# Kernel tuning notes

Measured on AMD Instinct MI355X. Metric: run time of the kernel, lower is better.

The kernel has to match this reference:

```python
import jax, jax.numpy as jnp
import numpy as np

F_IN, F_OUT, N_HEADS = 64, 256, 4
HEAD_DIM = F_OUT // N_HEADS


def setup_inputs() -> dict:
    key = jax.random.key(0)
    ks = jax.random.split(key, 9)
    s_in = 1.0 / np.sqrt(F_IN)
    s_out = 1.0 / np.sqrt(F_OUT)
    return {
        "x": jax.random.normal(ks[0], (4, 32, F_IN, 512), dtype=jnp.float32),
        "Wq": jax.random.normal(ks[1], (F_IN, F_OUT), dtype=jnp.float32) * s_in,
        "bq": jax.random.normal(ks[2], (F_OUT,), dtype=jnp.float32) * 0.01,
        "Wk": jax.random.normal(ks[3], (F_IN, F_OUT), dtype=jnp.float32) * s_in,
        "bk": jax.random.normal(ks[4], (F_OUT,), dtype=jnp.float32) * 0.01,
        "Wv": jax.random.normal(ks[5], (F_IN, F_OUT), dtype=jnp.float32) * s_in,
        "bv": jax.random.normal(ks[6], (F_OUT,), dtype=jnp.float32) * 0.01,
        "Wo": jax.random.normal(ks[7], (F_OUT, F_OUT), dtype=jnp.float32) * s_out,
        "bo": jax.random.normal(ks[8], (F_OUT,), dtype=jnp.float32) * 0.01,
    }


def reference(x, Wq, bq, Wk, bk, Wv, bv, Wo, bo):
    B, N, Fdim, T = x.shape
    xp = jnp.transpose(x, (0, 1, 3, 2))  # [B, N, T, F]
    q = xp @ Wq + bq  # [B, N, T, f_out]
    k = xp @ Wk + bk
    v = xp @ Wv + bv
    # split f_out into heads: [B, N, T, H, hd]
    q = q.reshape(B, N, T, N_HEADS, HEAD_DIM)
    k = k.reshape(B, N, T, N_HEADS, HEAD_DIM)
    v = v.reshape(B, N, T, N_HEADS, HEAD_DIM)
    scale = 1.0 / np.sqrt(HEAD_DIM)
    # full TxT score matrix per (batch, node, head), as in the original
    scores = jnp.einsum("bnqhd,bnkhd->bnhqk", q, k) * scale
    attn = jax.nn.softmax(scores, axis=-1)
    out = jnp.einsum("bnhqk,bnkhd->bnqhd", attn, v)  # [B, N, T, H, hd]
    out = out.reshape(B, N, T, F_OUT)  # head-concat along feature dim
    out = out @ Wo + bo  # fc_out; dropout is identity at inference
    return jnp.transpose(out, (0, 1, 3, 2))  # [B, N, f_out, T]
```

## Files before the change

kernel.cpp:

```cpp
#include <hip/hip_runtime.h>

constexpr int kT = 512;
constexpr int kF = 64;
constexpr int kC = 256;
constexpr int kH = 4;
constexpr int kHD = 64;
constexpr int kBN = 128;

typedef __attribute__((ext_vector_type(4))) float f32x4;
typedef __attribute__((ext_vector_type(8))) short s16x8;
typedef __attribute__((ext_vector_type(4))) unsigned int u32x4;

__device__ inline unsigned short f2bf(float f) {
  unsigned int u = __float_as_uint(f);
  u += 0x7fff + ((u >> 16) & 1);
  return (unsigned short)(u >> 16);
}

__device__ inline float max3f(float a, float b, float c) {
  return fmaxf(fmaxf(a, b), c);
}

__device__ inline float exp2_hw(float x) {
  float r;
  asm("v_exp_f32 %0, %1" : "=v"(r) : "v"(x));
  return r;
}

__global__ __launch_bounds__(256) void k_prep(
    const float* __restrict__ Wq, const float* __restrict__ Wk,
    const float* __restrict__ Wv, const float* __restrict__ Wo,
    unsigned short* __restrict__ WB, unsigned short* __restrict__ WoT) {
  int i = blockIdx.x * 256 + threadIdx.x;
  const int total = 768 * 64 + 256 * 256;
  for (; i < total; i += gridDim.x * 256) {
    if (i < 768 * 64) {
      int c = i >> 6, f = i & 63;
      int arr = c >> 8, cc = c & 255;
      const float* W = (arr == 0) ? Wq : (arr == 1) ? Wk : Wv;
      WB[i] = f2bf(W[f * 256 + cc]);
    } else {
      int j = i - 768 * 64;
      int co = j >> 8, c = j & 255;
      WoT[j] = f2bf(Wo[c * 256 + co]);
    }
  }
}

__global__ __launch_bounds__(256) void k_qkv(
    const float* __restrict__ x, const unsigned short* __restrict__ WB,
    const float* __restrict__ bq, const float* __restrict__ bk,
    const float* __restrict__ bv,
    unsigned short* __restrict__ Qw, unsigned short* __restrict__ Kw,
    unsigned short* __restrict__ Vw, int bn0) {
  __shared__ __align__(16) unsigned short shm[9216];

  const int tid = threadIdx.x;
  const int lbn = blockIdx.x >> 2;
  const int tch = blockIdx.x & 3;
  const float* xb = x + (size_t)(bn0 + lbn) * kF * kT + tch * 128;

  for (int idx = tid; idx < 2048; idx += 256) {
    int f = idx >> 5, t4 = idx & 31;
    float4 v = *(const float4*)(xb + f * kT + t4 * 4);
    shm[(t4 * 4 + 0) * 72 + f] = f2bf(v.x);
    shm[(t4 * 4 + 1) * 72 + f] = f2bf(v.y);
    shm[(t4 * 4 + 2) * 72 + f] = f2bf(v.z);
    shm[(t4 * 4 + 3) * 72 + f] = f2bf(v.w);
  }
  __syncthreads();

  const int lane = tid & 63, wid = tid >> 6;
  const int lr = lane & 15, lg = lane >> 4;

  s16x8 bfr[8][2];
#pragma unroll
  for (int tj = 0; tj < 8; ++tj)
#pragma unroll
    for (int kk = 0; kk < 2; ++kk)
      bfr[tj][kk] = *(const s16x8*)&shm[(tj * 16 + lr) * 72 + kk * 32 + lg * 8];
  __syncthreads();

  const float kQscale = 0.180336880111120426f;

  for (int i = 0; i < 12; ++i) {
    const int ci = wid * 12 + i;
    const int c0 = ci * 16;
    s16x8 af0 = *(const s16x8*)(WB + (size_t)(c0 + lr) * 64 + lg * 8);
    s16x8 af1 = *(const s16x8*)(WB + (size_t)(c0 + lr) * 64 + 32 + lg * 8);

    f32x4 acc[8];
#pragma unroll
    for (int tj = 0; tj < 8; ++tj) {
      f32x4 a = {0.f, 0.f, 0.f, 0.f};
      a = __builtin_amdgcn_mfma_f32_16x16x32_bf16(af0, bfr[tj][0], a, 0, 0, 0);
      a = __builtin_amdgcn_mfma_f32_16x16x32_bf16(af1, bfr[tj][1], a, 0, 0, 0);
      acc[tj] = a;
    }

    const int arr = c0 >> 8;
    const int h = (c0 & 255) >> 6;
    const int dbase0 = (c0 & 63);
    const int dbase = dbase0 + lg * 4;
    const float* bsrc = (arr == 0) ? bq : (arr == 1) ? bk : bv;
    float b0 = bsrc[h * 64 + dbase + 0];
    float b1 = bsrc[h * 64 + dbase + 1];
    float b2 = bsrc[h * 64 + dbase + 2];
    float b3 = bsrc[h * 64 + dbase + 3];

    if (arr < 2) {
      const float scale = (arr == 0) ? kQscale : 1.0f;
      unsigned short* dst = ((arr == 0) ? Qw : Kw) +
                            (size_t)(lbn * kH + h) * kT * kHD;
#pragma unroll
      for (int tj = 0; tj < 8; ++tj) {
        int t = tch * 128 + tj * 16 + lr;
        float v0 = (acc[tj][0] + b0) * scale;
        float v1 = (acc[tj][1] + b1) * scale;
        float v2 = (acc[tj][2] + b2) * scale;
        float v3 = (acc[tj][3] + b3) * scale;
        unsigned long long pk =
            (unsigned long long)f2bf(v0) |
            ((unsigned long long)f2bf(v1) << 16) |
            ((unsigned long long)f2bf(v2) << 32) |
            ((unsigned long long)f2bf(v3) << 48);
        *(unsigned long long*)(dst + (size_t)t * kHD + dbase) = pk;
      }
    } else {
      unsigned short* buf = shm + wid * (16 * 144);
#pragma unroll
      for (int tj = 0; tj < 8; ++tj) {
        buf[(lg * 4 + 0) * 144 + tj * 16 + lr] = f2bf(acc[tj][0] + b0);
        buf[(lg * 4 + 1) * 144 + tj * 16 + lr] = f2bf(acc[tj][1] + b1);
        buf[(lg * 4 + 2) * 144 + tj * 16 + lr] = f2bf(acc[tj][2] + b2);
        buf[(lg * 4 + 3) * 144 + tj * 16 + lr] = f2bf(acc[tj][3] + b3);
      }
      asm volatile("s_waitcnt lgkmcnt(0)" ::: "memory");
      unsigned short* dst = Vw + (size_t)(lbn * kH + h) * kHD * kT;
      const int row = lane >> 2, cc = lane & 3;
#pragma unroll
      for (int q4 = 0; q4 < 4; ++q4) {
        uint4 vv = *(const uint4*)&buf[row * 144 + (q4 * 4 + cc) * 8];
        *(uint4*)(dst + (size_t)(dbase0 + row) * kT + tch * 128 +
                  (q4 * 4 + cc) * 8) = vv;
      }
    }
  }
}

__global__ __launch_bounds__(1024, 4) void k_attn(
    const unsigned short* __restrict__ Qw, const unsigned short* __restrict__ Kw,
    const unsigned short* __restrict__ Vw, unsigned short* __restrict__ Aw) {
  __shared__ __align__(16) unsigned char KlB[512 * 128];
  __shared__ __align__(16) unsigned char VtB[64 * 1024];

  const int tid = threadIdx.x;
  const int lbn = blockIdx.x >> 2;
  const int h = blockIdx.x & 3;
  const size_t hb = (size_t)(lbn * kH + h) * kT * kHD;

  const uint4* Ksrc = (const uint4*)(Kw + hb);
#pragma unroll
  for (int i = 0; i < 4; ++i) {
    int cidx = tid + i * 1024;
    int t = cidx >> 3, c8 = cidx & 7;
    *(uint4*)(KlB + ((t * 128 + c8 * 16) ^ ((t & 7) << 4))) = Ksrc[cidx];
  }
  const unsigned short* Vs = Vw + hb;
#pragma unroll
  for (int i = 0; i < 8; ++i) {
    int gi = tid + i * 1024;
    int d = gi >> 7, gr = gi & 127;
    int b32 = gr >> 3, g2 = gr & 7;
    int hh = g2 >> 1, e = g2 & 1;
    uint2 v = *(const uint2*)(Vs + d * 512 + b32 * 32 + e * 16 + hh * 4);
    *(uint2*)(VtB + ((d * 1024 + gr * 8) ^ ((d & 7) << 4))) = v;
  }
  __syncthreads();

  const int lane = tid & 63, wid = tid >> 6;
  const int lr = lane & 15, lg = lane >> 4;
  const int swz = (lr & 7) << 4;
  const unsigned short* Qb = Qw + hb;
  unsigned short* Ab = Aw + (size_t)lbn * kT * kC + h * kHD;

  const int qbase = wid * 32;
  s16x8 qf[2][2];
#pragma unroll
  for (int qt = 0; qt < 2; ++qt) {
    qf[qt][0] = *(const s16x8*)(Qb + (size_t)(qbase + qt * 16 + lr) * kHD + lg * 8);
    qf[qt][1] = *(const s16x8*)(Qb + (size_t)(qbase + qt * 16 + lr) * kHD + 32 + lg * 8);
  }

  f32x4 o0[4] = {{0,0,0,0},{0,0,0,0},{0,0,0,0},{0,0,0,0}};
  f32x4 o1[4] = {{0,0,0,0},{0,0,0,0},{0,0,0,0},{0,0,0,0}};
  float m0 = -3e38f, m1 = -3e38f, l0 = 0.f, l1 = 0.f;

  const int koff = (lg * 16) ^ swz;
  const unsigned char* kp0 = KlB + lr * 128 + koff;
  const unsigned char* kp1 = KlB + lr * 128 + (koff ^ 64);
  const int voff = (lg * 16) ^ swz;
  const unsigned char* vp0 = VtB + lr * 1024 + voff;
  const unsigned char* vp1 = VtB + lr * 1024 + (voff ^ 64);

  unsigned int w0[8], w1[8];

#define SOFTMAX_QT(sa, m, l, o, w)                                            \
  {                                                                           \
    float g0 = max3f(sa[0][0], sa[0][1], sa[0][2]);                           \
    float g1 = max3f(sa[0][3], sa[1][0], sa[1][1]);                           \
    float g2 = max3f(sa[1][2], sa[1][3], sa[2][0]);                           \
    float g3 = max3f(sa[2][1], sa[2][2], sa[2][3]);                           \
    float g4 = max3f(sa[3][0], sa[3][1], sa[3][2]);                           \
    float tm = fmaxf(max3f(g0, g1, g2), max3f(g3, g4, sa[3][3]));             \
    if (__any(tm > m + 8.0f)) {                                               \
      tm = fmaxf(tm, __shfl_xor(tm, 16));                                     \
      tm = fmaxf(tm, __shfl_xor(tm, 32));                                     \
      float mn = fmaxf(m, tm);                                                \
      float al = exp2_hw(m - mn);                                             \
      m = mn;                                                                 \
      l *= al;                                                                \
      float aq0 = __shfl(al, (lane & 48) | (lg * 4 + 0));                     \
      float aq1 = __shfl(al, (lane & 48) | (lg * 4 + 1));                     \
      float aq2 = __shfl(al, (lane & 48) | (lg * 4 + 2));                     \
      float aq3 = __shfl(al, (lane & 48) | (lg * 4 + 3));                     \
      _Pragma("unroll")                                                       \
      for (int dt = 0; dt < 4; ++dt) {                                        \
        o[dt][0] *= aq0; o[dt][1] *= aq1;                                     \
        o[dt][2] *= aq2; o[dt][3] *= aq3;                                     \
      }                                                                       \
    }                                                                         \
    _Pragma("unroll")                                                         \
    for (int s = 0; s < 4; ++s) {                                             \
      float e0 = exp2_hw(sa[s][0] - m);                                       \
      float e1 = exp2_hw(sa[s][1] - m);                                       \
      float e2 = exp2_hw(sa[s][2] - m);                                       \
      float e3 = exp2_hw(sa[s][3] - m);                                       \
      l += (e0 + e1) + (e2 + e3);                                             \
      asm("v_cvt_pk_bf16_f32 %0, %1, %2" : "=v"(w[2*s]) : "v"(e0), "v"(e1));  \
      asm("v_cvt_pk_bf16_f32 %0, %1, %2" : "=v"(w[2*s+1]) : "v"(e2), "v"(e3));\
    }                                                                         \
  }

  for (int kc = 0; kc < 8; ++kc) {
    f32x4 sa0[4], sa1[4];
#pragma unroll
    for (int s = 0; s < 4; ++s) {
      s16x8 kf0 = *(const s16x8*)(kp0 + s * 2048);
      s16x8 kf1 = *(const s16x8*)(kp1 + s * 2048);
      f32x4 z0 = {0.f, 0.f, 0.f, 0.f};
      z0 = __builtin_amdgcn_mfma_f32_16x16x32_bf16(kf0, qf[0][0], z0, 0, 0, 0);
      z0 = __builtin_amdgcn_mfma_f32_16x16x32_bf16(kf1, qf[0][1], z0, 0, 0, 0);
      sa0[s] = z0;
      f32x4 z1 = {0.f, 0.f, 0.f, 0.f};
      z1 = __builtin_amdgcn_mfma_f32_16x16x32_bf16(kf0, qf[1][0], z1, 0, 0, 0);
      z1 = __builtin_amdgcn_mfma_f32_16x16x32_bf16(kf1, qf[1][1], z1, 0, 0, 0);
      sa1[s] = z1;
    }
    kp0 += 8192;
    kp1 += 8192;

    SOFTMAX_QT(sa0, m0, l0, o0, w0)
    SOFTMAX_QT(sa1, m1, l1, o1, w1)

    s16x8 pa00 = __builtin_bit_cast(s16x8, (u32x4){w0[0], w0[1], w0[2], w0[3]});
    s16x8 pa01 = __builtin_bit_cast(s16x8, (u32x4){w0[4], w0[5], w0[6], w0[7]});
    s16x8 pa10 = __builtin_bit_cast(s16x8, (u32x4){w1[0], w1[1], w1[2], w1[3]});
    s16x8 pa11 = __builtin_bit_cast(s16x8, (u32x4){w1[4], w1[5], w1[6], w1[7]});

#pragma unroll
    for (int dt = 0; dt < 4; ++dt) {
      s16x8 vb = *(const s16x8*)(vp0 + dt * 16384);
      o0[dt] = __builtin_amdgcn_mfma_f32_16x16x32_bf16(pa00, vb, o0[dt], 0, 0, 0);
      o1[dt] = __builtin_amdgcn_mfma_f32_16x16x32_bf16(pa10, vb, o1[dt], 0, 0, 0);
    }
#pragma unroll
    for (int dt = 0; dt < 4; ++dt) {
      s16x8 vb = *(const s16x8*)(vp1 + dt * 16384);
      o0[dt] = __builtin_amdgcn_mfma_f32_16x16x32_bf16(pa01, vb, o0[dt], 0, 0, 0);
      o1[dt] = __builtin_amdgcn_mfma_f32_16x16x32_bf16(pa11, vb, o1[dt], 0, 0, 0);
    }
    vp0 += 128;
    vp1 += 128;
  }
#undef SOFTMAX_QT

#pragma unroll
  for (int qt = 0; qt < 2; ++qt) {
    float l = (qt == 0) ? l0 : l1;
    f32x4* o = (qt == 0) ? o0 : o1;
    float l2 = l + __shfl_xor(l, 16);
    float lr4 = l2 + __shfl_xor(l2, 32);
    float li0 = 1.0f / __shfl(lr4, (lane & 48) | (lg * 4 + 0));
    float li1 = 1.0f / __shfl(lr4, (lane & 48) | (lg * 4 + 1));
    float li2 = 1.0f / __shfl(lr4, (lane & 48) | (lg * 4 + 2));
    float li3 = 1.0f / __shfl(lr4, (lane & 48) | (lg * 4 + 3));
    const int qb = qbase + qt * 16;
#pragma unroll
    for (int r = 0; r < 4; ++r) {
      float li = (r == 0) ? li0 : (r == 1) ? li1 : (r == 2) ? li2 : li3;
      unsigned short* orow = Ab + (size_t)(qb + lg * 4 + r) * kC;
#pragma unroll
      for (int dt = 0; dt < 4; ++dt)
        orow[dt * 16 + lr] = f2bf(o[dt][r] * li);
    }
  }
}

__global__ __launch_bounds__(512) void k_proj(
    const unsigned short* __restrict__ Aw, const unsigned short* __restrict__ WoT,
    const float* __restrict__ bo, float* __restrict__ out, int bn0) {
  __shared__ __align__(16) unsigned char Al[128 * 512];

  const int tid = threadIdx.x;
  const int lbn = blockIdx.x >> 2;
  const int tch = blockIdx.x & 3;
  const int t0 = tch * 128;

  const uint4* Asrc = (const uint4*)(Aw + ((size_t)lbn * kT + t0) * kC);
#pragma unroll
  for (int i = 0; i < 8; ++i) {
    int idx = tid + i * 512;
    int trow = idx >> 5, cc = idx & 31;
    *(uint4*)(Al + ((trow * 512 + cc * 16) ^ ((trow & 7) << 4))) = Asrc[idx];
  }
  __syncthreads();

  const int lane = tid & 63, wid = tid >> 6;
  const int lr = lane & 15, lg = lane >> 4;
  const int swz = (lr & 7) << 4;
  const int tb = (wid >> 2) * 64;
  const int cob = (wid & 3) * 64;

  float* ob = out + (size_t)(bn0 + lbn) * kC * kT;

  for (int ci = 0; ci < 4; ++ci) {
    const int co0 = cob + ci * 16;
    s16x8 af[8];
#pragma unroll
    for (int kc = 0; kc < 8; ++kc)
      af[kc] = *(const s16x8*)(WoT + (size_t)(co0 + lr) * 256 + kc * 32 + lg * 8);
    float b4[4];
#pragma unroll
    for (int r = 0; r < 4; ++r) b4[r] = bo[co0 + lg * 4 + r];

#pragma unroll
    for (int tj = 0; tj < 4; ++tj) {
      const unsigned char* ap = Al + (tb + tj * 16 + lr) * 512;
      f32x4 acc = {0.f, 0.f, 0.f, 0.f};
#pragma unroll
      for (int kc = 0; kc < 8; ++kc) {
        s16x8 bfr = *(const s16x8*)(ap + ((kc * 64 + lg * 16) ^ swz));
        acc = __builtin_amdgcn_mfma_f32_16x16x32_bf16(af[kc], bfr, acc, 0, 0, 0);
      }
      int t = t0 + tb + tj * 16 + lr;
#pragma unroll
      for (int r = 0; r < 4; ++r)
        ob[(size_t)(co0 + lg * 4 + r) * kT + t] = acc[r] + b4[r];
    }
  }
}

extern "C" void kernel_launch(void* const* d_in, const int* in_sizes, int n_in,
                              void* d_out, int out_size, void* d_ws, size_t ws_size,
                              hipStream_t stream) {
  const float* x  = (const float*)d_in[0];
  const float* Wq = (const float*)d_in[1];
  const float* bq = (const float*)d_in[2];
  const float* Wk = (const float*)d_in[3];
  const float* bk = (const float*)d_in[4];
  const float* Wv = (const float*)d_in[5];
  const float* bv = (const float*)d_in[6];
  const float* Wo = (const float*)d_in[7];
  const float* bo = (const float*)d_in[8];
  float* out = (float*)d_out;

  const size_t wElems = 768 * 64 + 256 * 256;
  const size_t perbn = (size_t)4 * kT * kC * 2;
  if (ws_size < wElems * 2 + perbn) return;
  int cap = (int)((ws_size - wElems * 2) / perbn);
  if (cap > kBN) cap = kBN;

  unsigned short* WB  = (unsigned short*)d_ws;
  unsigned short* WoT = WB + 768 * 64;
  unsigned short* Q = WB + wElems;
  unsigned short* K = Q + (size_t)cap * kT * kC;
  unsigned short* V = K + (size_t)cap * kT * kC;
  unsigned short* A = V + (size_t)cap * kT * kC;

  k_prep<<<dim3(448), dim3(256), 0, stream>>>(Wq, Wk, Wv, Wo, WB, WoT);

  for (int s = 0; s < kBN; s += cap) {
    int nb = (kBN - s < cap) ? (kBN - s) : cap;
    k_qkv<<<dim3(nb * 4), dim3(256), 0, stream>>>(x, WB, bq, bk, bv,
                                                  Q, K, V, s);
    k_attn<<<dim3(nb * 4), dim3(1024), 0, stream>>>(Q, K, V, A);
    k_proj<<<dim3(nb * 4), dim3(512), 0, stream>>>(A, WoT, bo, out, s);
  }
}
```

Baseline: 134.0 us.

## Read K fragments directly from global memory and give each wave 64 queries

The attention kernel drops the K staging buffer in shared memory and loads K fragments straight from global memory through L2/L1. It also halves the block to 512 threads, so each wave handles 64 query rows instead of 32 and reuses each K and V fragment across four query tiles. This removes the K staging pass and halves LDS use. In exchange, register pressure rises from the larger accumulator set, and the global K loads are exposed inside the loop.

```diff
diff --git a/kernel.cpp b/kernel.cpp
--- a/kernel.cpp
+++ b/kernel.cpp
@@ -148,10 +148,9 @@
   }
 }
 
-__global__ __launch_bounds__(1024, 4) void k_attn(
+__global__ __launch_bounds__(512, 2) void k_attn(
     const unsigned short* __restrict__ Qw, const unsigned short* __restrict__ Kw,
     const unsigned short* __restrict__ Vw, unsigned short* __restrict__ Aw) {
-  __shared__ __align__(16) unsigned char KlB[512 * 128];
   __shared__ __align__(16) unsigned char VtB[64 * 1024];
 
   const int tid = threadIdx.x;
@@ -159,17 +158,10 @@
   const int h = blockIdx.x & 3;
   const size_t hb = (size_t)(lbn * kH + h) * kT * kHD;
 
-  const uint4* Ksrc = (const uint4*)(Kw + hb);
-#pragma unroll
-  for (int i = 0; i < 4; ++i) {
-    int cidx = tid + i * 1024;
-    int t = cidx >> 3, c8 = cidx & 7;
-    *(uint4*)(KlB + ((t * 128 + c8 * 16) ^ ((t & 7) << 4))) = Ksrc[cidx];
-  }
   const unsigned short* Vs = Vw + hb;
 #pragma unroll
-  for (int i = 0; i < 8; ++i) {
-    int gi = tid + i * 1024;
+  for (int i = 0; i < 16; ++i) {
+    int gi = tid + i * 512;
     int d = gi >> 7, gr = gi & 127;
     int b32 = gr >> 3, g2 = gr & 7;
     int hh = g2 >> 1, e = g2 & 1;
@@ -184,112 +176,110 @@
   const unsigned short* Qb = Qw + hb;
   unsigned short* Ab = Aw + (size_t)lbn * kT * kC + h * kHD;
 
-  const int qbase = wid * 32;
-  s16x8 qf[2][2];
-#pragma unroll
-  for (int qt = 0; qt < 2; ++qt) {
+  const int qbase = wid * 64;
+  s16x8 qf[4][2];
+#pragma unroll
+  for (int qt = 0; qt < 4; ++qt) {
     qf[qt][0] = *(const s16x8*)(Qb + (size_t)(qbase + qt * 16 + lr) * kHD + lg * 8);
     qf[qt][1] = *(const s16x8*)(Qb + (size_t)(qbase + qt * 16 + lr) * kHD + 32 + lg * 8);
   }
 
-  f32x4 o0[4] = {{0,0,0,0},{0,0,0,0},{0,0,0,0},{0,0,0,0}};
-  f32x4 o1[4] = {{0,0,0,0},{0,0,0,0},{0,0,0,0},{0,0,0,0}};
-  float m0 = -3e38f, m1 = -3e38f, l0 = 0.f, l1 = 0.f;
-
-  const int koff = (lg * 16) ^ swz;
-  const unsigned char* kp0 = KlB + lr * 128 + koff;
-  const unsigned char* kp1 = KlB + lr * 128 + (koff ^ 64);
-  const int voff = (lg * 16) ^ swz;
-  const unsigned char* vp0 = VtB + lr * 1024 + voff;
-  const unsigned char* vp1 = VtB + lr * 1024 + (voff ^ 64);
-
-  unsigned int w0[8], w1[8];
-
-#define SOFTMAX_QT(sa, m, l, o, w)                                            \
-  {                                                                           \
-    float g0 = max3f(sa[0][0], sa[0][1], sa[0][2]);                           \
-    float g1 = max3f(sa[0][3], sa[1][0], sa[1][1]);                           \
-    float g2 = max3f(sa[1][2], sa[1][3], sa[2][0]);                           \
-    float g3 = max3f(sa[2][1], sa[2][2], sa[2][3]);                           \
-    float g4 = max3f(sa[3][0], sa[3][1], sa[3][2]);                           \
-    float tm = fmaxf(max3f(g0, g1, g2), max3f(g3, g4, sa[3][3]));             \
-    if (__any(tm > m + 8.0f)) {                                               \
-      tm = fmaxf(tm, __shfl_xor(tm, 16));                                     \
-      tm = fmaxf(tm, __shfl_xor(tm, 32));                                     \
-      float mn = fmaxf(m, tm);                                                \
-      float al = exp2_hw(m - mn);                                             \
-      m = mn;                                                                 \
-      l *= al;                                                                \
-      float aq0 = __shfl(al, (lane & 48) | (lg * 4 + 0));                     \
-      float aq1 = __shfl(al, (lane & 48) | (lg * 4 + 1));                     \
-      float aq2 = __shfl(al, (lane & 48) | (lg * 4 + 2));                     \
-      float aq3 = __shfl(al, (lane & 48) | (lg * 4 + 3));                     \
-      _Pragma("unroll")                                                       \
-      for (int dt = 0; dt < 4; ++dt) {                                        \
-        o[dt][0] *= aq0; o[dt][1] *= aq1;                                     \
-        o[dt][2] *= aq2; o[dt][3] *= aq3;                                     \
-      }                                                                       \
-    }                                                                         \
-    _Pragma("unroll")                                                         \
-    for (int s = 0; s < 4; ++s) {                                             \
-      float e0 = exp2_hw(sa[s][0] - m);                                       \
-      float e1 = exp2_hw(sa[s][1] - m);                                       \
-      float e2 = exp2_hw(sa[s][2] - m);                                       \
-      float e3 = exp2_hw(sa[s][3] - m);                                       \
-      l += (e0 + e1) + (e2 + e3);                                             \
-      asm("v_cvt_pk_bf16_f32 %0, %1, %2" : "=v"(w[2*s]) : "v"(e0), "v"(e1));  \
-      asm("v_cvt_pk_bf16_f32 %0, %1, %2" : "=v"(w[2*s+1]) : "v"(e2), "v"(e3));\
-    }                                                                         \
-  }
+  f32x4 o[4][4] = {{{0,0,0,0},{0,0,0,0},{0,0,0,0},{0,0,0,0}},
+                   {{0,0,0,0},{0,0,0,0},{0,0,0,0},{0,0,0,0}},
+                   {{0,0,0,0},{0,0,0,0},{0,0,0,0},{0,0,0,0}},
+                   {{0,0,0,0},{0,0,0,0},{0,0,0,0},{0,0,0,0}}};
+  float l[4] = {0.f, 0.f, 0.f, 0.f};
+  float m[4] = {-3e38f, -3e38f, -3e38f, -3e38f};
+
+  const unsigned short* kg = Kw + hb + lr * kHD + lg * 8;
+  const unsigned char* vp0 = VtB + lr * 1024 + ((lg * 16) ^ swz);
+  const unsigned char* vp1 = VtB + lr * 1024 + (((lg * 16) ^ 64) ^ swz);
 
   for (int kc = 0; kc < 8; ++kc) {
-    f32x4 sa0[4], sa1[4];
+    const unsigned short* kgc = kg + kc * 64 * kHD;
+    s16x8 kf0[4], kf1[4];
 #pragma unroll
     for (int s = 0; s < 4; ++s) {
-      s16x8 kf0 = *(const s16x8*)(kp0 + s * 2048);
-      s16x8 kf1 = *(const s16x8*)(kp1 + s * 2048);
-      f32x4 z0 = {0.f, 0.f, 0.f, 0.f};
-      z0 = __builtin_amdgcn_mfma_f32_16x16x32_bf16(kf0, qf[0][0], z0, 0, 0, 0);
-      z0 = __builtin_amdgcn_mfma_f32_16x16x32_bf16(kf1, qf[0][1], z0, 0, 0, 0);
-      sa0[s] = z0;
-      f32x4 z1 = {0.f, 0.f, 0.f, 0.f};
-      z1 = __builtin_amdgcn_mfma_f32_16x16x32_bf16(kf0, qf[1][0], z1, 0, 0, 0);
-      z1 = __builtin_amdgcn_mfma_f32_16x16x32_bf16(kf1, qf[1][1], z1, 0, 0, 0);
-      sa1[s] = z1;
-    }
-    kp0 += 8192;
-    kp1 += 8192;
-
-    SOFTMAX_QT(sa0, m0, l0, o0, w0)
-    SOFTMAX_QT(sa1, m1, l1, o1, w1)
-
-    s16x8 pa00 = __builtin_bit_cast(s16x8, (u32x4){w0[0], w0[1], w0[2], w0[3]});
-    s16x8 pa01 = __builtin_bit_cast(s16x8, (u32x4){w0[4], w0[5], w0[6], w0[7]});
-    s16x8 pa10 = __builtin_bit_cast(s16x8, (u32x4){w1[0], w1[1], w1[2], w1[3]});
-    s16x8 pa11 = __builtin_bit_cast(s16x8, (u32x4){w1[4], w1[5], w1[6], w1[7]});
+      kf0[s] = *(const s16x8*)(kgc + s * 16 * kHD);
+      kf1[s] = *(const s16x8*)(kgc + s * 16 * kHD + 32);
+    }
+
+    f32x4 sa[4][4];
+#pragma unroll
+    for (int qt = 0; qt < 4; ++qt)
+#pragma unroll
+      for (int s = 0; s < 4; ++s) {
+        f32x4 z = {0.f, 0.f, 0.f, 0.f};
+        z = __builtin_amdgcn_mfma_f32_16x16x32_bf16(kf0[s], qf[qt][0], z, 0, 0, 0);
+        z = __builtin_amdgcn_mfma_f32_16x16x32_bf16(kf1[s], qf[qt][1], z, 0, 0, 0);
+        sa[qt][s] = z;
+      }
+
+    s16x8 pa[4][2];
+#pragma unroll
+    for (int qt = 0; qt < 4; ++qt) {
+      float g0 = max3f(sa[qt][0][0], sa[qt][0][1], sa[qt][0][2]);
+      float g1 = max3f(sa[qt][0][3], sa[qt][1][0], sa[qt][1][1]);
+      float g2 = max3f(sa[qt][1][2], sa[qt][1][3], sa[qt][2][0]);
+      float g3 = max3f(sa[qt][2][1], sa[qt][2][2], sa[qt][2][3]);
+      float g4 = max3f(sa[qt][3][0], sa[qt][3][1], sa[qt][3][2]);
+      float tm = fmaxf(max3f(g0, g1, g2), max3f(g3, g4, sa[qt][3][3]));
+      if (__any(tm > m[qt] + 8.0f)) {
+        tm = fmaxf(tm, __shfl_xor(tm, 16));
+        tm = fmaxf(tm, __shfl_xor(tm, 32));
+        float mn = fmaxf(m[qt], tm);
+        float al = exp2_hw(m[qt] - mn);
+        m[qt] = mn;
+        l[qt] *= al;
+        float aq0 = __shfl(al, (lane & 48) | (lg * 4 + 0));
+        float aq1 = __shfl(al, (lane & 48) | (lg * 4 + 1));
+        float aq2 = __shfl(al, (lane & 48) | (lg * 4 + 2));
+        float aq3 = __shfl(al, (lane & 48) | (lg * 4 + 3));
+#pragma unroll
+        for (int dt = 0; dt < 4; ++dt) {
+          o[qt][dt][0] *= aq0; o[qt][dt][1] *= aq1;
+          o[qt][dt][2] *= aq2; o[qt][dt][3] *= aq3;
+        }
+      }
+      unsigned int w[8];
+#pragma unroll
+      for (int s = 0; s < 4; ++s) {
+        float e0 = exp2_hw(sa[qt][s][0] - m[qt]);
+        float e1 = exp2_hw(sa[qt][s][1] - m[qt]);
+        float e2 = exp2_hw(sa[qt][s][2] - m[qt]);
+        float e3 = exp2_hw(sa[qt][s][3] - m[qt]);
+        l[qt] += (e0 + e1) + (e2 + e3);
+        asm("v_cvt_pk_bf16_f32 %0, %1, %2" : "=v"(w[2*s])   : "v"(e0), "v"(e1));
+        asm("v_cvt_pk_bf16_f32 %0, %1, %2" : "=v"(w[2*s+1]) : "v"(e2), "v"(e3));
+      }
+      pa[qt][0] = __builtin_bit_cast(s16x8, (u32x4){w[0], w[1], w[2], w[3]});
+      pa[qt][1] = __builtin_bit_cast(s16x8, (u32x4){w[4], w[5], w[6], w[7]});
+    }
 
 #pragma unroll
     for (int dt = 0; dt < 4; ++dt) {
       s16x8 vb = *(const s16x8*)(vp0 + dt * 16384);
-      o0[dt] = __builtin_amdgcn_mfma_f32_16x16x32_bf16(pa00, vb, o0[dt], 0, 0, 0);
-      o1[dt] = __builtin_amdgcn_mfma_f32_16x16x32_bf16(pa10, vb, o1[dt], 0, 0, 0);
+#pragma unroll
+      for (int qt = 0; qt < 4; ++qt)
+        o[qt][dt] = __builtin_amdgcn_mfma_f32_16x16x32_bf16(pa[qt][0], vb,
+                                                            o[qt][dt], 0, 0, 0);
     }
 #pragma unroll
     for (int dt = 0; dt < 4; ++dt) {
       s16x8 vb = *(const s16x8*)(vp1 + dt * 16384);
-      o0[dt] = __builtin_amdgcn_mfma_f32_16x16x32_bf16(pa01, vb, o0[dt], 0, 0, 0);
-      o1[dt] = __builtin_amdgcn_mfma_f32_16x16x32_bf16(pa11, vb, o1[dt], 0, 0, 0);
+#pragma unroll
+      for (int qt = 0; qt < 4; ++qt)
+        o[qt][dt] = __builtin_amdgcn_mfma_f32_16x16x32_bf16(pa[qt][1], vb,
+                                                            o[qt][dt], 0, 0, 0);
     }
     vp0 += 128;
     vp1 += 128;
   }
-#undef SOFTMAX_QT
-
-#pragma unroll
-  for (int qt = 0; qt < 2; ++qt) {
-    float l = (qt == 0) ? l0 : l1;
-    f32x4* o = (qt == 0) ? o0 : o1;
-    float l2 = l + __shfl_xor(l, 16);
+
+#pragma unroll
+  for (int qt = 0; qt < 4; ++qt) {
+    float lq = l[qt];
+    float l2 = lq + __shfl_xor(lq, 16);
     float lr4 = l2 + __shfl_xor(l2, 32);
     float li0 = 1.0f / __shfl(lr4, (lane & 48) | (lg * 4 + 0));
     float li1 = 1.0f / __shfl(lr4, (lane & 48) | (lg * 4 + 1));
@@ -302,7 +292,7 @@
       unsigned short* orow = Ab + (size_t)(qb + lg * 4 + r) * kC;
 #pragma unroll
       for (int dt = 0; dt < 4; ++dt)
-        orow[dt * 16 + lr] = f2bf(o[dt][r] * li);
+        orow[dt * 16 + lr] = f2bf(o[qt][dt][r] * li);
     }
   }
 }
@@ -394,7 +384,7 @@
     int nb = (kBN - s < cap) ? (kBN - s) : cap;
     k_qkv<<<dim3(nb * 4), dim3(256), 0, stream>>>(x, WB, bq, bk, bv,
                                                   Q, K, V, s);
-    k_attn<<<dim3(nb * 4), dim3(1024), 0, stream>>>(Q, K, V, A);
+    k_attn<<<dim3(nb * 4), dim3(512), 0, stream>>>(Q, K, V, A);
     k_proj<<<dim3(nb * 4), dim3(512), 0, stream>>>(A, WoT, bo, out, s);
   }
 }
```

New measurement: 136.1 us. No clear change (+1.6%).

## Fuse QKV projection into attention kernel, computing K/V directly into LDS

Applied to the files above, without the earlier changes.

Merges the QKV projection kernel into the attention kernel. Each (bn, head) block loads x in four time chunks, computes K and V for its head straight into swizzled shared memory and Q into registers, which removes the global Q/K/V workspace round trip and one launch. It also drops the capacity-based chunk loop so all batch-nodes run in two launches. In exchange, x is re-read and converted once per head (4x redundant x loads and projection work), LDS use per block grows to about 146KB, and the V writes become scattered 2-byte LDS stores.

```diff
diff --git a/kernel.cpp b/kernel.cpp
--- a/kernel.cpp
+++ b/kernel.cpp
@@ -47,161 +47,149 @@
   }
 }
 
-__global__ __launch_bounds__(256) void k_qkv(
+__global__ __launch_bounds__(1024, 4) void k_fattn(
     const float* __restrict__ x, const unsigned short* __restrict__ WB,
     const float* __restrict__ bq, const float* __restrict__ bk,
-    const float* __restrict__ bv,
-    unsigned short* __restrict__ Qw, unsigned short* __restrict__ Kw,
-    unsigned short* __restrict__ Vw, int bn0) {
-  __shared__ __align__(16) unsigned short shm[9216];
+    const float* __restrict__ bv, unsigned short* __restrict__ Aw) {
+  __shared__ __align__(16) unsigned char smem[149504];
+  unsigned char* Kl = smem;
+  unsigned char* VtB = smem + 65536;
+  unsigned short* xC = (unsigned short*)(smem + 131072);
 
   const int tid = threadIdx.x;
   const int lbn = blockIdx.x >> 2;
-  const int tch = blockIdx.x & 3;
-  const float* xb = x + (size_t)(bn0 + lbn) * kF * kT + tch * 128;
-
-  for (int idx = tid; idx < 2048; idx += 256) {
-    int f = idx >> 5, t4 = idx & 31;
-    float4 v = *(const float4*)(xb + f * kT + t4 * 4);
-    shm[(t4 * 4 + 0) * 72 + f] = f2bf(v.x);
-    shm[(t4 * 4 + 1) * 72 + f] = f2bf(v.y);
-    shm[(t4 * 4 + 2) * 72 + f] = f2bf(v.z);
-    shm[(t4 * 4 + 3) * 72 + f] = f2bf(v.w);
-  }
-  __syncthreads();
-
+  const int h = blockIdx.x & 3;
   const int lane = tid & 63, wid = tid >> 6;
   const int lr = lane & 15, lg = lane >> 4;
-
-  s16x8 bfr[8][2];
-#pragma unroll
-  for (int tj = 0; tj < 8; ++tj)
-#pragma unroll
-    for (int kk = 0; kk < 2; ++kk)
-      bfr[tj][kk] = *(const s16x8*)&shm[(tj * 16 + lr) * 72 + kk * 32 + lg * 8];
-  __syncthreads();
+  const int swz = (lr & 7) << 4;
 
   const float kQscale = 0.180336880111120426f;
-
-  for (int i = 0; i < 12; ++i) {
-    const int ci = wid * 12 + i;
-    const int c0 = ci * 16;
-    s16x8 af0 = *(const s16x8*)(WB + (size_t)(c0 + lr) * 64 + lg * 8);
-    s16x8 af1 = *(const s16x8*)(WB + (size_t)(c0 + lr) * 64 + 32 + lg * 8);
-
-    f32x4 acc[8];
-#pragma unroll
-    for (int tj = 0; tj < 8; ++tj) {
+  const unsigned short* WBq = WB + (size_t)(h * 64) * 64;
+  const unsigned short* WBk = WB + (size_t)(256 + h * 64) * 64;
+  const unsigned short* WBv = WB + (size_t)(512 + h * 64) * 64;
+
+  s16x8 qf[2][2];
+
+  for (int tch = 0; tch < 4; ++tch) {
+    __syncthreads();
+    const float* xb = x + (size_t)lbn * kF * kT + tch * 128;
+#pragma unroll
+    for (int it = 0; it < 2; ++it) {
+      int idx = tid + it * 1024;
+      int f = idx >> 5, t4 = idx & 31;
+      float4 v = *(const float4*)(xb + f * kT + t4 * 4);
+      xC[(t4 * 4 + 0) * 72 + f] = f2bf(v.x);
+      xC[(t4 * 4 + 1) * 72 + f] = f2bf(v.y);
+      xC[(t4 * 4 + 2) * 72 + f] = f2bf(v.z);
+      xC[(t4 * 4 + 3) * 72 + f] = f2bf(v.w);
+    }
+    __syncthreads();
+
+#pragma unroll
+    for (int j = 0; j < 4; ++j) {
+      const int tau = wid * 4 + j;
+      const int isV = tau >> 5;
+      const int tl = tau & 31;
+      const int ct = tl >> 3, tt = tl & 7;
+      const unsigned short* Wsrc = isV ? WBv : WBk;
+      s16x8 af0 = *(const s16x8*)(Wsrc + (ct * 16 + lr) * 64 + lg * 8);
+      s16x8 af1 = *(const s16x8*)(Wsrc + (ct * 16 + lr) * 64 + 32 + lg * 8);
+      s16x8 bf0 = *(const s16x8*)&xC[(tt * 16 + lr) * 72 + lg * 8];
+      s16x8 bf1 = *(const s16x8*)&xC[(tt * 16 + lr) * 72 + 32 + lg * 8];
       f32x4 a = {0.f, 0.f, 0.f, 0.f};
-      a = __builtin_amdgcn_mfma_f32_16x16x32_bf16(af0, bfr[tj][0], a, 0, 0, 0);
-      a = __builtin_amdgcn_mfma_f32_16x16x32_bf16(af1, bfr[tj][1], a, 0, 0, 0);
-      acc[tj] = a;
-    }
-
-    const int arr = c0 >> 8;
-    const int h = (c0 & 255) >> 6;
-    const int dbase0 = (c0 & 63);
-    const int dbase = dbase0 + lg * 4;
-    const float* bsrc = (arr == 0) ? bq : (arr == 1) ? bk : bv;
-    float b0 = bsrc[h * 64 + dbase + 0];
-    float b1 = bsrc[h * 64 + dbase + 1];
-    float b2 = bsrc[h * 64 + dbase + 2];
-    float b3 = bsrc[h * 64 + dbase + 3];
-
-    if (arr < 2) {
-      const float scale = (arr == 0) ? kQscale : 1.0f;
-      unsigned short* dst = ((arr == 0) ? Qw : Kw) +
-                            (size_t)(lbn * kH + h) * kT * kHD;
-#pragma unroll
-      for (int tj = 0; tj < 8; ++tj) {
-        int t = tch * 128 + tj * 16 + lr;
-        float v0 = (acc[tj][0] + b0) * scale;
-        float v1 = (acc[tj][1] + b1) * scale;
-        float v2 = (acc[tj][2] + b2) * scale;
-        float v3 = (acc[tj][3] + b3) * scale;
+      a = __builtin_amdgcn_mfma_f32_16x16x32_bf16(af0, bf0, a, 0, 0, 0);
+      a = __builtin_amdgcn_mfma_f32_16x16x32_bf16(af1, bf1, a, 0, 0, 0);
+      const float* bsrc = isV ? bv : bk;
+      const int dbase = ct * 16 + lg * 4;
+      const int t = tch * 128 + tt * 16 + lr;
+      float v0 = a[0] + bsrc[h * 64 + dbase + 0];
+      float v1 = a[1] + bsrc[h * 64 + dbase + 1];
+      float v2 = a[2] + bsrc[h * 64 + dbase + 2];
+      float v3 = a[3] + bsrc[h * 64 + dbase + 3];
+      if (!isV) {
         unsigned long long pk =
             (unsigned long long)f2bf(v0) |
             ((unsigned long long)f2bf(v1) << 16) |
             ((unsigned long long)f2bf(v2) << 32) |
             ((unsigned long long)f2bf(v3) << 48);
-        *(unsigned long long*)(dst + (size_t)t * kHD + dbase) = pk;
-      }
-    } else {
-      unsigned short* buf = shm + wid * (16 * 144);
-#pragma unroll
-      for (int tj = 0; tj < 8; ++tj) {
-        buf[(lg * 4 + 0) * 144 + tj * 16 + lr] = f2bf(acc[tj][0] + b0);
-        buf[(lg * 4 + 1) * 144 + tj * 16 + lr] = f2bf(acc[tj][1] + b1);
-        buf[(lg * 4 + 2) * 144 + tj * 16 + lr] = f2bf(acc[tj][2] + b2);
-        buf[(lg * 4 + 3) * 144 + tj * 16 + lr] = f2bf(acc[tj][3] + b3);
-      }
-      asm volatile("s_waitcnt lgkmcnt(0)" ::: "memory");
-      unsigned short* dst = Vw + (size_t)(lbn * kH + h) * kHD * kT;
-      const int row = lane >> 2, cc = lane & 3;
-#pragma unroll
-      for (int q4 = 0; q4 < 4; ++q4) {
-        uint4 vv = *(const uint4*)&buf[row * 144 + (q4 * 4 + cc) * 8];
-        *(uint4*)(dst + (size_t)(dbase0 + row) * kT + tch * 128 +
-                  (q4 * 4 + cc) * 8) = vv;
-      }
-    }
-  }
-}
-
-__global__ __launch_bounds__(1024, 4) void k_attn(
-    const unsigned short* __restrict__ Qw, const unsigned short* __restrict__ Kw,
-    const unsigned short* __restrict__ Vw, unsigned short* __restrict__ Aw) {
-  __shared__ __align__(16) unsigned char KlB[512 * 128];
-  __shared__ __align__(16) unsigned char VtB[64 * 1024];
-
-  const int tid = threadIdx.x;
-  const int lbn = blockIdx.x >> 2;
-  const int h = blockIdx.x & 3;
-  const size_t hb = (size_t)(lbn * kH + h) * kT * kHD;
-
-  const uint4* Ksrc = (const uint4*)(Kw + hb);
-#pragma unroll
-  for (int i = 0; i < 4; ++i) {
-    int cidx = tid + i * 1024;
-    int t = cidx >> 3, c8 = cidx & 7;
-    *(uint4*)(KlB + ((t * 128 + c8 * 16) ^ ((t & 7) << 4))) = Ksrc[cidx];
-  }
-  const unsigned short* Vs = Vw + hb;
-#pragma unroll
-  for (int i = 0; i < 8; ++i) {
-    int gi = tid + i * 1024;
-    int d = gi >> 7, gr = gi & 127;
-    int b32 = gr >> 3, g2 = gr & 7;
-    int hh = g2 >> 1, e = g2 & 1;
-    uint2 v = *(const uint2*)(Vs + d * 512 + b32 * 32 + e * 16 + hh * 4);
-    *(uint2*)(VtB + ((d * 1024 + gr * 8) ^ ((d & 7) << 4))) = v;
+        *(unsigned long long*)(Kl + ((t * 128 + dbase * 2) ^ ((t & 7) << 4))) = pk;
+      } else {
+        const int pos = ((t >> 5) << 5) | (((t >> 2) & 3) << 3) |
+                        (((t >> 4) & 1) << 2) | (t & 3);
+        const unsigned short pv[4] = {f2bf(v0), f2bf(v1), f2bf(v2), f2bf(v3)};
+#pragma unroll
+        for (int r = 0; r < 4; ++r) {
+          const int d = dbase + r;
+          *(unsigned short*)(VtB + ((d * 1024 + pos * 2) ^ ((d & 7) << 4))) = pv[r];
+        }
+      }
+    }
+
+    const bool qown = ((wid >> 2) == tch);
+    f32x4 qa[2][4];
+    if (qown) {
+#pragma unroll
+      for (int qt = 0; qt < 2; ++qt) {
+        const int ttq = (wid & 3) * 2 + qt;
+#pragma unroll
+        for (int ct = 0; ct < 4; ++ct) {
+          s16x8 af0 = *(const s16x8*)(WBq + (ct * 16 + lr) * 64 + lg * 8);
+          s16x8 af1 = *(const s16x8*)(WBq + (ct * 16 + lr) * 64 + 32 + lg * 8);
+          s16x8 bf0 = *(const s16x8*)&xC[(ttq * 16 + lr) * 72 + lg * 8];
+          s16x8 bf1 = *(const s16x8*)&xC[(ttq * 16 + lr) * 72 + 32 + lg * 8];
+          f32x4 a = {0.f, 0.f, 0.f, 0.f};
+          a = __builtin_amdgcn_mfma_f32_16x16x32_bf16(af0, bf0, a, 0, 0, 0);
+          a = __builtin_amdgcn_mfma_f32_16x16x32_bf16(af1, bf1, a, 0, 0, 0);
+          qa[qt][ct] = a;
+        }
+      }
+    }
+    __syncthreads();
+    if (qown) {
+#pragma unroll
+      for (int qt = 0; qt < 2; ++qt) {
+        const int qrow = (wid & 3) * 32 + qt * 16 + lr;
+#pragma unroll
+        for (int ct = 0; ct < 4; ++ct) {
+          f32x4 a = qa[qt][ct];
+          const int dbase = ct * 16 + lg * 4;
+          float q0 = (a[0] + bq[h * 64 + dbase + 0]) * kQscale;
+          float q1 = (a[1] + bq[h * 64 + dbase + 1]) * kQscale;
+          float q2 = (a[2] + bq[h * 64 + dbase + 2]) * kQscale;
+          float q3 = (a[3] + bq[h * 64 + dbase + 3]) * kQscale;
+          unsigned long long pk =
+              (unsigned long long)f2bf(q0) |
+              ((unsigned long long)f2bf(q1) << 16) |
+              ((unsigned long long)f2bf(q2) << 32) |
+              ((unsigned long long)f2bf(q3) << 48);
+          *(unsigned long long*)&xC[qrow * 72 + dbase] = pk;
+        }
+      }
+    }
+    __syncthreads();
+    if (qown) {
+#pragma unroll
+      for (int qt = 0; qt < 2; ++qt) {
+        const int qrow = (wid & 3) * 32 + qt * 16 + lr;
+        qf[qt][0] = *(const s16x8*)&xC[qrow * 72 + lg * 8];
+        qf[qt][1] = *(const s16x8*)&xC[qrow * 72 + 32 + lg * 8];
+      }
+    }
   }
   __syncthreads();
 
-  const int lane = tid & 63, wid = tid >> 6;
-  const int lr = lane & 15, lg = lane >> 4;
-  const int swz = (lr & 7) << 4;
-  const unsigned short* Qb = Qw + hb;
   unsigned short* Ab = Aw + (size_t)lbn * kT * kC + h * kHD;
-
   const int qbase = wid * 32;
-  s16x8 qf[2][2];
-#pragma unroll
-  for (int qt = 0; qt < 2; ++qt) {
-    qf[qt][0] = *(const s16x8*)(Qb + (size_t)(qbase + qt * 16 + lr) * kHD + lg * 8);
-    qf[qt][1] = *(const s16x8*)(Qb + (size_t)(qbase + qt * 16 + lr) * kHD + 32 + lg * 8);
-  }
 
   f32x4 o0[4] = {{0,0,0,0},{0,0,0,0},{0,0,0,0},{0,0,0,0}};
   f32x4 o1[4] = {{0,0,0,0},{0,0,0,0},{0,0,0,0},{0,0,0,0}};
   float m0 = -3e38f, m1 = -3e38f, l0 = 0.f, l1 = 0.f;
 
   const int koff = (lg * 16) ^ swz;
-  const unsigned char* kp0 = KlB + lr * 128 + koff;
-  const unsigned char* kp1 = KlB + lr * 128 + (koff ^ 64);
-  const int voff = (lg * 16) ^ swz;
-  const unsigned char* vp0 = VtB + lr * 1024 + voff;
-  const unsigned char* vp1 = VtB + lr * 1024 + (voff ^ 64);
+  const unsigned char* kp0 = Kl + lr * 128 + koff;
+  const unsigned char* kp1 = Kl + lr * 128 + (koff ^ 64);
+  const unsigned char* vp0 = VtB + lr * 1024 + ((lg * 16) ^ swz);
+  const unsigned char* vp1 = VtB + lr * 1024 + (((lg * 16) ^ 64) ^ swz);
 
   unsigned int w0[8], w1[8];
 
@@ -309,7 +297,7 @@
 
 __global__ __launch_bounds__(512) void k_proj(
     const unsigned short* __restrict__ Aw, const unsigned short* __restrict__ WoT,
-    const float* __restrict__ bo, float* __restrict__ out, int bn0) {
+    const float* __restrict__ bo, float* __restrict__ out) {
   __shared__ __align__(16) unsigned char Al[128 * 512];
 
   const int tid = threadIdx.x;
@@ -332,7 +320,7 @@
   const int tb = (wid >> 2) * 64;
   const int cob = (wid & 3) * 64;
 
-  float* ob = out + (size_t)(bn0 + lbn) * kC * kT;
+  float* ob = out + (size_t)lbn * kC * kT;
 
   for (int ci = 0; ci < 4; ++ci) {
     const int co0 = cob + ci * 16;
@@ -376,25 +364,14 @@
   float* out = (float*)d_out;
 
   const size_t wElems = 768 * 64 + 256 * 256;
-  const size_t perbn = (size_t)4 * kT * kC * 2;
-  if (ws_size < wElems * 2 + perbn) return;
-  int cap = (int)((ws_size - wElems * 2) / perbn);
-  if (cap > kBN) cap = kBN;
+  const size_t aBytes = (size_t)kBN * kT * kC * 2;
+  if (ws_size < wElems * 2 + aBytes) return;
 
   unsigned short* WB  = (unsigned short*)d_ws;
   unsigned short* WoT = WB + 768 * 64;
-  unsigned short* Q = WB + wElems;
-  unsigned short* K = Q + (size_t)cap * kT * kC;
-  unsigned short* V = K + (size_t)cap * kT * kC;
-  unsigned short* A = V + (size_t)cap * kT * kC;
+  unsigned short* A   = WB + wElems;
 
   k_prep<<<dim3(448), dim3(256), 0, stream>>>(Wq, Wk, Wv, Wo, WB, WoT);
-
-  for (int s = 0; s < kBN; s += cap) {
-    int nb = (kBN - s < cap) ? (kBN - s) : cap;
-    k_qkv<<<dim3(nb * 4), dim3(256), 0, stream>>>(x, WB, bq, bk, bv,
-                                                  Q, K, V, s);
-    k_attn<<<dim3(nb * 4), dim3(1024), 0, stream>>>(Q, K, V, A);
-    k_proj<<<dim3(nb * 4), dim3(512), 0, stream>>>(A, WoT, bo, out, s);
-  }
-}
+  k_fattn<<<dim3(kBN * kH), dim3(1024), 0, stream>>>(x, WB, bq, bk, bv, A);
+  k_proj<<<dim3(kBN * 4), dim3(512), 0, stream>>>(A, WoT, bo, out);
+}
```

After: 126.5 us. 5.6% less time.
